# Kernel tuning notes

Hardware: AMD Instinct MI355X
Metric: run time of the kernel (lower is better)

The kernel has to match this reference:

```python
import jax, jax.numpy as jnp
import numpy as np


def _silu(v):
    return v * jax.nn.sigmoid(v)


def setup_inputs() -> dict:
    key = jax.random.key(0)
    ks = jax.random.split(key, 12)
    B, N, DS = 4, 12500, 63      # batch, nodes per graph, dim_single
    E = 800000                   # total edges (avg degree 16)
    BN = B * N
    ND = DS + 1                  # node_dim = dim_single + 1 (timestep channel)
    H, ED = 128, 32              # hidden_dim, edge_dim (fixed in __init__)
    MIN = 2 * ND + ED            # m_input feature dim = 160

    def lin(k, i, o):
        return (jax.random.normal(k, (i, o)) / np.sqrt(i)).astype(jnp.float32)

    return {
        "x": jax.random.normal(ks[0], (B, N, 3), dtype=jnp.float32) * 5.0,
        "cond": jax.random.normal(ks[1], (B, N, DS), dtype=jnp.float32),
        "edge_dist": jax.random.uniform(ks[2], (E,), dtype=jnp.float32) * 15.0,
        "ew1": lin(ks[3], 1, ED), "eb1": jnp.zeros((ED,), jnp.float32),
        "ew2": lin(ks[4], ED, ED), "eb2": jnp.zeros((ED,), jnp.float32),
        "nw1": lin(ks[5], MIN, H), "nb1": jnp.zeros((H,), jnp.float32),
        "nw2": lin(ks[6], H, ND), "nb2": jnp.zeros((ND,), jnp.float32),
        "cw1": lin(ks[7], MIN, H), "cb1": jnp.zeros((H,), jnp.float32),
        "cw2": lin(ks[8], H, 1),
        "edge_index": jax.random.randint(ks[9], (2, E), 0, BN, dtype=jnp.int64 if jax.config.jax_enable_x64 else jnp.int32),
        "t": 100,
    }


def reference(x, cond, edge_dist, ew1, eb1, ew2, eb2, nw1, nb1, nw2, nb2,
              cw1, cb1, cw2, edge_index, t):
    B, N, _ = x.shape
    BN = B * N
    # append timestep scalar channel to conditioning -> node features h
    t_feat = jnp.full((B, N, 1), t, dtype=x.dtype)
    h = jnp.concatenate([cond, t_feat], axis=-1).reshape(BN, -1)   # [BN, node_dim]
    xf = x.reshape(BN, 3)

    src, dst = edge_index[0], edge_index[1]
    # edge_mlp on scalar distances -> [E, edge_dim]
    edge_attr = _silu(edge_dist[:, None] @ ew1 + eb1) @ ew2 + eb2
    # gather + concat -> [E, 2*node_dim + edge_dim]
    m_input = jnp.concatenate([h[src], h[dst], edge_attr], axis=-1)
    # node_mlp (its output h_agg is discarded by p_sample, kept for faithfulness)
    m = _silu(m_input @ nw1 + nb1) @ nw2 + nb2
    h_agg = jax.ops.segment_sum(m, dst, num_segments=BN)
    h_out = h + h_agg  # unused by p_sample's return
    del h_out
    # coord_mlp -> scalar weight per edge
    coord_weight = _silu(m_input @ cw1 + cb1) @ cw2                 # [E, 1]
    dir_vec = xf[src] - xf[dst]                                     # [E, 3]
    dir_len = jnp.maximum(jnp.linalg.norm(dir_vec, axis=-1, keepdims=True), 1e-8)
    coord_update = coord_weight * (dir_vec / dir_len)
    x_agg = jax.ops.segment_sum(coord_update, dst, num_segments=BN)
    return (xf + x_agg).reshape(B, N, 3)
```

## Files before the change

### kernel.cpp

```cpp
#include <hip/hip_runtime.h>
#include <hip/hip_bf16.h>

typedef __attribute__((ext_vector_type(8))) short bf16x8;
typedef __attribute__((ext_vector_type(4))) float f32x4;
typedef __attribute__((ext_vector_type(4), aligned(4))) float f32x4u;
typedef __attribute__((ext_vector_type(2), aligned(4))) float f32x2u;

__device__ __forceinline__ unsigned short f2bf(float f) {
    unsigned int u = __float_as_uint(f);
    unsigned int r = (u + 0x7fffu + ((u >> 16) & 1u)) >> 16;
    return (unsigned short)r;
}
__device__ __forceinline__ float bflo(unsigned int u) { return __uint_as_float(u << 16); }
__device__ __forceinline__ float bfhi(unsigned int u) { return __uint_as_float(u & 0xffff0000u); }

__global__ void init_out_kernel(const float* __restrict__ x, float* __restrict__ out, int n) {
    int i = blockIdx.x * blockDim.x + threadIdx.x;
    if (i < n) out[i] = x[i];
}

__global__ void prep_bt2_kernel(const float* __restrict__ cw1, unsigned short* __restrict__ bt2) {
    int idx = blockIdx.x * 256 + threadIdx.x;
    if (idx < 256 * 64) {
        int n = idx >> 6, k = idx & 63;
        float v = 0.f;
        if (k < 63) v = (n < 128) ? cw1[k * 128 + n] : cw1[(64 + k) * 128 + (n - 128)];
        bt2[n * 64 + k] = f2bf(v);
    }
}

__global__ void prep_consts_kernel(const float* __restrict__ ew2, const float* __restrict__ eb2,
                                   const float* __restrict__ cw1, const float* __restrict__ cb1,
                                   const int* __restrict__ tptr,
                                   unsigned short* __restrict__ bt_M, float* __restrict__ c0) {
    int j = threadIdx.x;
    float t = (float)tptr[0];
    float cacc = cb1[j] + t * (cw1[63 * 128 + j] + cw1[127 * 128 + j]);
    float m[32];
    #pragma unroll
    for (int p = 0; p < 32; ++p) m[p] = 0.f;
    for (int i = 0; i < 32; ++i) {
        float w = cw1[(128 + i) * 128 + j];
        cacc = fmaf(eb2[i], w, cacc);
        #pragma unroll
        for (int p = 0; p < 32; ++p) m[p] = fmaf(ew2[p * 32 + i], w, m[p]);
    }
    c0[j] = cacc;
    #pragma unroll
    for (int p = 0; p < 32; ++p) bt_M[j * 32 + p] = f2bf(m[p]);
}

__device__ __forceinline__ bf16x8 load8_bf(const float* p) {
    f32x4u a = *(const f32x4u*)p;
    f32x4u b = *(const f32x4u*)(p + 4);
    bf16x8 r;
    r[0] = f2bf(a[0]); r[1] = f2bf(a[1]); r[2] = f2bf(a[2]); r[3] = f2bf(a[3]);
    r[4] = f2bf(b[0]); r[5] = f2bf(b[1]); r[6] = f2bf(b[2]); r[7] = f2bf(b[3]);
    return r;
}
__device__ __forceinline__ bf16x8 load7z_bf(const float* p) {
    f32x4u a = *(const f32x4u*)p;
    f32x2u b = *(const f32x2u*)(p + 4);
    float c = p[6];
    bf16x8 r;
    r[0] = f2bf(a[0]); r[1] = f2bf(a[1]); r[2] = f2bf(a[2]); r[3] = f2bf(a[3]);
    r[4] = f2bf(b[0]); r[5] = f2bf(b[1]); r[6] = f2bf(c);  r[7] = 0;
    return r;
}

__global__ __launch_bounds__(256) void prep_uv_kernel(
    const float* __restrict__ cond, const unsigned short* __restrict__ bt2,
    unsigned short* __restrict__ UV, int BN)
{
    const int tid = threadIdx.x, lane = tid & 63, wid = tid >> 6;
    const int fr = lane & 15, kq = lane >> 4;
    int node = blockIdx.x * 64 + wid * 16 + fr;
    if (node >= BN) node = BN - 1;

    const float* cp = cond + (long)node * 63;
    bf16x8 b0 = load8_bf(cp + 8 * kq);
    bf16x8 b1 = (kq < 3) ? load8_bf(cp + 32 + 8 * kq) : load7z_bf(cp + 56);

    char* UVb = (char*)UV;
    const unsigned off = ((unsigned)node * 256u + (unsigned)(kq * 4)) * 2u;

    #pragma unroll
    for (int n = 0; n < 16; ++n) {
        bf16x8 a0 = *reinterpret_cast<const bf16x8*>(&bt2[(n * 16 + fr) * 64 + 8 * kq]);
        bf16x8 a1 = *reinterpret_cast<const bf16x8*>(&bt2[(n * 16 + fr) * 64 + 32 + 8 * kq]);
        f32x4 acc = (f32x4){0.f, 0.f, 0.f, 0.f};
        acc = __builtin_amdgcn_mfma_f32_16x16x32_bf16(a0, b0, acc, 0, 0, 0);
        acc = __builtin_amdgcn_mfma_f32_16x16x32_bf16(a1, b1, acc, 0, 0, 0);
        uint2 pk;
        pk.x = (unsigned)f2bf(acc[0]) | ((unsigned)f2bf(acc[1]) << 16);
        pk.y = (unsigned)f2bf(acc[2]) | ((unsigned)f2bf(acc[3]) << 16);
        *reinterpret_cast<uint2*>(UVb + off + n * 32) = pk;
    }
}

__global__ __launch_bounds__(256, 4) void edge_kernel(
    const float* __restrict__ x, const float* __restrict__ edge_dist,
    const float* __restrict__ ew1, const float* __restrict__ eb1,
    const unsigned short* __restrict__ bt_M, const float* __restrict__ c0f,
    const float* __restrict__ cw2, const unsigned short* __restrict__ UV,
    const int* __restrict__ edge_index, float* __restrict__ out, int E)
{
    __shared__ __align__(16) unsigned short s_lds[128][40];
    __shared__ int srcl[128];
    __shared__ int dstl[128];
    __shared__ float cw_lds[128];

    const int tid = threadIdx.x, lane = tid & 63, wid = tid >> 6;
    const int fr = lane & 15, kq = lane >> 4;
    const int e0 = blockIdx.x * 128;

    if (tid < 128) {
        int e = e0 + tid; if (e >= E) e = E - 1;
        float dist = edge_dist[e];
        #pragma unroll
        for (int i = 0; i < 16; ++i) {
            float v0 = fmaf(dist, ew1[2 * i],     eb1[2 * i]);
            float v1 = fmaf(dist, ew1[2 * i + 1], eb1[2 * i + 1]);
            float s0 = v0 / (1.f + __expf(-v0));
            float s1 = v1 / (1.f + __expf(-v1));
            unsigned pk = (unsigned)f2bf(s0) | ((unsigned)f2bf(s1) << 16);
            *reinterpret_cast<unsigned*>(&s_lds[tid][2 * i]) = pk;
        }
    } else {
        int r = tid - 128;
        int e = e0 + r; if (e >= E) e = E - 1;
        srcl[r] = edge_index[e];
        dstl[r] = edge_index[E + e];
    }
    __syncthreads();

    bf16x8 sb[2];
    #pragma unroll
    for (int m = 0; m < 2; ++m)
        sb[m] = *reinterpret_cast<const bf16x8*>(&s_lds[wid * 32 + m * 16 + fr][8 * kq]);

    unsigned bu[2], bv[2];
    #pragma unroll
    for (int m = 0; m < 2; ++m) {
        int row = wid * 32 + m * 16 + fr;
        bu[m] = (unsigned)srcl[row] * 512u + (unsigned)(kq * 8);
        bv[m] = (unsigned)dstl[row] * 512u + 256u + (unsigned)(kq * 8);
    }

    const char* UVb = (const char*)UV;
    float psum[2] = {0.f, 0.f};

    #pragma unroll 1
    for (int nh = 0; nh < 2; ++nh) {
        f32x4 acc[2][4];
        #pragma unroll
        for (int n = 0; n < 4; ++n) {
            f32x4u c = *reinterpret_cast<const f32x4u*>(c0f + (nh * 4 + n) * 16 + kq * 4);
            acc[0][n] = (f32x4){c[0], c[1], c[2], c[3]};
            acc[1][n] = acc[0][n];
        }
        #pragma unroll
        for (int n = 0; n < 4; ++n) {
            bf16x8 aw = *reinterpret_cast<const bf16x8*>(&bt_M[((nh * 4 + n) * 16 + fr) * 32 + 8 * kq]);
            acc[0][n] = __builtin_amdgcn_mfma_f32_16x16x32_bf16(aw, sb[0], acc[0][n], 0, 0, 0);
            acc[1][n] = __builtin_amdgcn_mfma_f32_16x16x32_bf16(aw, sb[1], acc[1][n], 0, 0, 0);
        }
        #pragma unroll
        for (int n = 0; n < 4; ++n) {
            f32x4u w2 = *reinterpret_cast<const f32x4u*>(cw2 + (nh * 4 + n) * 16 + kq * 4);
            const int cb = (nh * 4 + n) * 32;
            #pragma unroll
            for (int m = 0; m < 2; ++m) {
                uint2 uu = *reinterpret_cast<const uint2*>(UVb + bu[m] + cb);
                uint2 vv = *reinterpret_cast<const uint2*>(UVb + bv[m] + cb);
                float uf[4] = {bflo(uu.x), bfhi(uu.x), bflo(uu.y), bfhi(uu.y)};
                float vf[4] = {bflo(vv.x), bfhi(vv.x), bflo(vv.y), bfhi(vv.y)};
                #pragma unroll
                for (int r = 0; r < 4; ++r) {
                    float h = acc[m][n][r] + uf[r] + vf[r];
                    float sil = h / (1.f + __expf(-h));
                    psum[m] = fmaf(sil, w2[r], psum[m]);
                }
            }
        }
    }

    #pragma unroll
    for (int m = 0; m < 2; ++m) {
        psum[m] += __shfl_xor(psum[m], 16, 64);
        psum[m] += __shfl_xor(psum[m], 32, 64);
    }
    if (kq == 0) {
        #pragma unroll
        for (int m = 0; m < 2; ++m)
            cw_lds[wid * 32 + m * 16 + fr] = psum[m];
    }
    __syncthreads();

    if (tid < 128) {
        int e = e0 + tid;
        if (e < E) {
            float coord_w = cw_lds[tid];
            int src = srcl[tid];
            int dst = dstl[tid];
            float dx = x[src * 3 + 0] - x[dst * 3 + 0];
            float dy = x[src * 3 + 1] - x[dst * 3 + 1];
            float dz = x[src * 3 + 2] - x[dst * 3 + 2];
            float len = sqrtf(fmaf(dx, dx, fmaf(dy, dy, dz * dz)));
            len = fmaxf(len, 1e-8f);
            float sc = coord_w / len;
            atomicAdd(&out[dst * 3 + 0], sc * dx);
            atomicAdd(&out[dst * 3 + 1], sc * dy);
            atomicAdd(&out[dst * 3 + 2], sc * dz);
        }
    }
}

extern "C" void kernel_launch(void* const* d_in, const int* in_sizes, int n_in,
                              void* d_out, int out_size, void* d_ws, size_t ws_size,
                              hipStream_t stream) {
    const float* x         = (const float*)d_in[0];
    const float* cond      = (const float*)d_in[1];
    const float* edge_dist = (const float*)d_in[2];
    const float* ew1       = (const float*)d_in[3];
    const float* eb1       = (const float*)d_in[4];
    const float* ew2       = (const float*)d_in[5];
    const float* eb2       = (const float*)d_in[6];
    const float* cw1       = (const float*)d_in[11];
    const float* cb1       = (const float*)d_in[12];
    const float* cw2       = (const float*)d_in[13];
    const int*   edge_index= (const int*)d_in[14];
    const int*   tptr      = (const int*)d_in[15];
    float* out = (float*)d_out;

    const int E  = in_sizes[2];
    const int BN = in_sizes[1] / 63;
    const int n_out = out_size;

    char* ws = (char*)d_ws;
    unsigned short* bt_M = (unsigned short*)(ws);
    float*          c0   = (float*)(ws + 8192);
    unsigned short* bt2  = (unsigned short*)(ws + 16384);
    unsigned short* UV   = (unsigned short*)(ws + 65536);

    init_out_kernel<<<(n_out + 255) / 256, 256, 0, stream>>>(x, out, n_out);
    prep_bt2_kernel<<<64, 256, 0, stream>>>(cw1, bt2);
    prep_consts_kernel<<<1, 128, 0, stream>>>(ew2, eb2, cw1, cb1, tptr, bt_M, c0);
    prep_uv_kernel<<<(BN + 63) / 64, 256, 0, stream>>>(cond, bt2, UV, BN);

    int blocks = (E + 127) / 128;
    edge_kernel<<<blocks, 256, 0, stream>>>(x, edge_dist, ew1, eb1,
                                            bt_M, c0, cw2, UV,
                                            edge_index, out, E);
}
```

Baseline: 286.7 us.

## Relayout UV rows per lane and prefetch gathered features as 16-byte loads

Changes the per-node UV table layout so each lane's slice of the U and V halves is contiguous, letting the edge kernel gather all needed source and destination features up front with eight 16-byte loads per row instead of many scattered 8-byte loads inside the loop. The nh loop is fully unrolled and the occupancy hint is lowered to 3 waves to make room for the extra registers. Separately, the three small setup kernels are merged into one launch to cut launch overhead. The cost is higher register pressure and lower occupancy in the edge kernel.

Result: slower. 303.5 us (+5.9%).

```diff
diff --git a/kernel.cpp b/kernel.cpp
--- a/kernel.cpp
+++ b/kernel.cpp
@@ -14,40 +14,42 @@
 __device__ __forceinline__ float bflo(unsigned int u) { return __uint_as_float(u << 16); }
 __device__ __forceinline__ float bfhi(unsigned int u) { return __uint_as_float(u & 0xffff0000u); }
 
-__global__ void init_out_kernel(const float* __restrict__ x, float* __restrict__ out, int n) {
-    int i = blockIdx.x * blockDim.x + threadIdx.x;
-    if (i < n) out[i] = x[i];
-}
-
-__global__ void prep_bt2_kernel(const float* __restrict__ cw1, unsigned short* __restrict__ bt2) {
-    int idx = blockIdx.x * 256 + threadIdx.x;
-    if (idx < 256 * 64) {
+__global__ void prep_merged_kernel(
+    const float* __restrict__ x, float* __restrict__ out, int n_out,
+    const float* __restrict__ cw1, unsigned short* __restrict__ bt2,
+    const float* __restrict__ ew2, const float* __restrict__ eb2,
+    const float* __restrict__ cb1, const int* __restrict__ tptr,
+    unsigned short* __restrict__ bt_M, float* __restrict__ c0)
+{
+    const int b = blockIdx.x, tid = threadIdx.x;
+    if (b < 64) {
+        int idx = b * 256 + tid;
         int n = idx >> 6, k = idx & 63;
         float v = 0.f;
         if (k < 63) v = (n < 128) ? cw1[k * 128 + n] : cw1[(64 + k) * 128 + (n - 128)];
         bt2[n * 64 + k] = f2bf(v);
-    }
-}
-
-__global__ void prep_consts_kernel(const float* __restrict__ ew2, const float* __restrict__ eb2,
-                                   const float* __restrict__ cw1, const float* __restrict__ cb1,
-                                   const int* __restrict__ tptr,
-                                   unsigned short* __restrict__ bt_M, float* __restrict__ c0) {
-    int j = threadIdx.x;
-    float t = (float)tptr[0];
-    float cacc = cb1[j] + t * (cw1[63 * 128 + j] + cw1[127 * 128 + j]);
-    float m[32];
-    #pragma unroll
-    for (int p = 0; p < 32; ++p) m[p] = 0.f;
-    for (int i = 0; i < 32; ++i) {
-        float w = cw1[(128 + i) * 128 + j];
-        cacc = fmaf(eb2[i], w, cacc);
-        #pragma unroll
-        for (int p = 0; p < 32; ++p) m[p] = fmaf(ew2[p * 32 + i], w, m[p]);
-    }
-    c0[j] = cacc;
-    #pragma unroll
-    for (int p = 0; p < 32; ++p) bt_M[j * 32 + p] = f2bf(m[p]);
+    } else if (b == 64) {
+        if (tid < 128) {
+            int j = tid;
+            float t = (float)tptr[0];
+            float cacc = cb1[j] + t * (cw1[63 * 128 + j] + cw1[127 * 128 + j]);
+            float m[32];
+            #pragma unroll
+            for (int p = 0; p < 32; ++p) m[p] = 0.f;
+            for (int i = 0; i < 32; ++i) {
+                float w = cw1[(128 + i) * 128 + j];
+                cacc = fmaf(eb2[i], w, cacc);
+                #pragma unroll
+                for (int p = 0; p < 32; ++p) m[p] = fmaf(ew2[p * 32 + i], w, m[p]);
+            }
+            c0[j] = cacc;
+            #pragma unroll
+            for (int p = 0; p < 32; ++p) bt_M[j * 32 + p] = f2bf(m[p]);
+        }
+    } else {
+        int i = (b - 65) * 256 + tid;
+        if (i < n_out) out[i] = x[i];
+    }
 }
 
 __device__ __forceinline__ bf16x8 load8_bf(const float* p) {
@@ -82,7 +84,7 @@
     bf16x8 b1 = (kq < 3) ? load8_bf(cp + 32 + 8 * kq) : load7z_bf(cp + 56);
 
     char* UVb = (char*)UV;
-    const unsigned off = ((unsigned)node * 256u + (unsigned)(kq * 4)) * 2u;
+    const unsigned nb = (unsigned)node * 512u + (unsigned)(kq * 64);
 
     #pragma unroll
     for (int n = 0; n < 16; ++n) {
@@ -94,11 +96,12 @@
         uint2 pk;
         pk.x = (unsigned)f2bf(acc[0]) | ((unsigned)f2bf(acc[1]) << 16);
         pk.y = (unsigned)f2bf(acc[2]) | ((unsigned)f2bf(acc[3]) << 16);
-        *reinterpret_cast<uint2*>(UVb + off + n * 32) = pk;
-    }
-}
-
-__global__ __launch_bounds__(256, 4) void edge_kernel(
+        unsigned off = nb + ((n & 8) ? 256u : 0u) + (unsigned)((n & 7) * 8);
+        *reinterpret_cast<uint2*>(UVb + off) = pk;
+    }
+}
+
+__global__ __launch_bounds__(256, 3) void edge_kernel(
     const float* __restrict__ x, const float* __restrict__ edge_dist,
     const float* __restrict__ ew1, const float* __restrict__ eb1,
     const unsigned short* __restrict__ bt_M, const float* __restrict__ c0f,
@@ -143,14 +146,22 @@
     #pragma unroll
     for (int m = 0; m < 2; ++m) {
         int row = wid * 32 + m * 16 + fr;
-        bu[m] = (unsigned)srcl[row] * 512u + (unsigned)(kq * 8);
-        bv[m] = (unsigned)dstl[row] * 512u + 256u + (unsigned)(kq * 8);
+        bu[m] = (unsigned)srcl[row] * 512u + (unsigned)(kq * 64);
+        bv[m] = (unsigned)dstl[row] * 512u + 256u + (unsigned)(kq * 64);
     }
 
     const char* UVb = (const char*)UV;
+    uint4 Lu[2][4], Lv[2][4];
+    #pragma unroll
+    for (int m = 0; m < 2; ++m)
+        #pragma unroll
+        for (int i = 0; i < 4; ++i) {
+            Lu[m][i] = *reinterpret_cast<const uint4*>(UVb + bu[m] + i * 16);
+            Lv[m][i] = *reinterpret_cast<const uint4*>(UVb + bv[m] + i * 16);
+        }
+
     float psum[2] = {0.f, 0.f};
-
-    #pragma unroll 1
+    #pragma unroll
     for (int nh = 0; nh < 2; ++nh) {
         f32x4 acc[2][4];
         #pragma unroll
@@ -167,14 +178,16 @@
         }
         #pragma unroll
         for (int n = 0; n < 4; ++n) {
-            f32x4u w2 = *reinterpret_cast<const f32x4u*>(cw2 + (nh * 4 + n) * 16 + kq * 4);
-            const int cb = (nh * 4 + n) * 32;
+            const int g = nh * 4 + n;
+            f32x4u w2 = *reinterpret_cast<const f32x4u*>(cw2 + g * 16 + kq * 4);
             #pragma unroll
             for (int m = 0; m < 2; ++m) {
-                uint2 uu = *reinterpret_cast<const uint2*>(UVb + bu[m] + cb);
-                uint2 vv = *reinterpret_cast<const uint2*>(UVb + bv[m] + cb);
-                float uf[4] = {bflo(uu.x), bfhi(uu.x), bflo(uu.y), bfhi(uu.y)};
-                float vf[4] = {bflo(vv.x), bfhi(vv.x), bflo(vv.y), bfhi(vv.y)};
+                unsigned du0 = (g & 1) ? Lu[m][g >> 1].z : Lu[m][g >> 1].x;
+                unsigned du1 = (g & 1) ? Lu[m][g >> 1].w : Lu[m][g >> 1].y;
+                unsigned dv0 = (g & 1) ? Lv[m][g >> 1].z : Lv[m][g >> 1].x;
+                unsigned dv1 = (g & 1) ? Lv[m][g >> 1].w : Lv[m][g >> 1].y;
+                float uf[4] = {bflo(du0), bfhi(du0), bflo(du1), bfhi(du1)};
+                float vf[4] = {bflo(dv0), bfhi(dv0), bflo(dv1), bfhi(dv1)};
                 #pragma unroll
                 for (int r = 0; r < 4; ++r) {
                     float h = acc[m][n][r] + uf[r] + vf[r];
@@ -243,9 +256,9 @@
     unsigned short* bt2  = (unsigned short*)(ws + 16384);
     unsigned short* UV   = (unsigned short*)(ws + 65536);
 
-    init_out_kernel<<<(n_out + 255) / 256, 256, 0, stream>>>(x, out, n_out);
-    prep_bt2_kernel<<<64, 256, 0, stream>>>(cw1, bt2);
-    prep_consts_kernel<<<1, 128, 0, stream>>>(ew2, eb2, cw1, cb1, tptr, bt_M, c0);
+    int init_blocks = (n_out + 255) / 256;
+    prep_merged_kernel<<<65 + init_blocks, 256, 0, stream>>>(
+        x, out, n_out, cw1, bt2, ew2, eb2, cb1, tptr, bt_M, c0);
     prep_uv_kernel<<<(BN + 63) / 64, 256, 0, stream>>>(cond, bt2, UV, BN);
 
     int blocks = (E + 127) / 128;
```
